# Kernel tuning notes

Hardware: AMD Instinct MI355X
Metric: run time of the kernel (lower is better)

Reference implementation:

```python
import jax, jax.numpy as jnp
import numpy as np

N_NODES = 50000
NNZ = 800000
NUM_EDGES = 10000
D = 128
EPS = 1e-8


def setup_inputs() -> dict:
    key = jax.random.key(0)
    k1, k2, k3, k4 = jax.random.split(key, 4)
    x = jax.random.normal(k1, (N_NODES, D), dtype=jnp.float32)
    node_ids = jax.random.randint(k2, (NNZ,), 0, N_NODES, dtype=jnp.int64)
    edge_ids = jax.random.randint(k3, (NNZ,), 0, NUM_EDGES, dtype=jnp.int64)
    hyperedge_index = jnp.stack([node_ids, edge_ids], axis=0)  # [2, nnz]
    # nn.Linear(in, out, bias=False) weight is [out, in]; kaiming-uniform-ish init
    bound = 1.0 / np.sqrt(D)
    W_node = jax.random.uniform(k4, (D, D), minval=-bound, maxval=bound, dtype=jnp.float32)
    bias = jnp.zeros((D,), dtype=jnp.float32)
    return {"x": x, "hyperedge_index": hyperedge_index, "W_node": W_node,
            "bias": bias, "num_hyperedges": NUM_EDGES}


def reference(x, hyperedge_index, W_node, bias, num_hyperedges):
    src = hyperedge_index[0]   # node ids, [nnz]
    edge = hyperedge_index[1]  # hyperedge ids, [nnz]
    N = x.shape[0]

    x_node = x @ W_node.T                                # [N, D]

    # node -> hyperedge mean
    edge_sum = jax.ops.segment_sum(x_node[src], edge, num_segments=num_hyperedges)
    node_counts = jax.ops.segment_sum(jnp.ones_like(edge, dtype=x.dtype), edge,
                                      num_segments=num_hyperedges)
    hyperedge_attr = edge_sum / (node_counts[:, None] + EPS)  # [E, D]

    # hyperedge -> node mean
    out = jax.ops.segment_sum(hyperedge_attr[edge], src, num_segments=N)
    degrees = jax.ops.segment_sum(jnp.ones_like(src, dtype=x.dtype), src,
                                  num_segments=N)
    out = out / (degrees[:, None] + EPS)                 # [N, D]

    return out + x_node + bias
```

## Files before the change

### kernel.cpp

```cpp
#include <hip/hip_runtime.h>

#define D 128
#define EPS 1e-8f
#define E_NUM 10000
#define CAP_E 192
#define CAP_N 64
#define CHUNK 2048
#define EB2 625
#define NB2 782
#define TB 1407
#define CAPB_E 1536
#define CAPB_N 1280
#define NODE_BASE (EB2 * CAPB_E)
#define STAGE_TOTAL (NODE_BASE + NB2 * CAPB_N)

typedef __attribute__((ext_vector_type(8))) short bf16x8;
typedef __attribute__((ext_vector_type(4))) float f32x4;

__device__ __forceinline__ unsigned bf16rn(float f) {
  unsigned u = __float_as_uint(f);
  return (u + 0x7fffu + ((u >> 16) & 1u)) >> 16;
}
__device__ __forceinline__ unsigned bf16pack(float a, float b) {
  return bf16rn(a) | (bf16rn(b) << 16);
}
__device__ __forceinline__ float lof(unsigned u) { return __uint_as_float(u << 16); }
__device__ __forceinline__ float hif(unsigned u) { return __uint_as_float(u & 0xffff0000u); }

#define ACCQ(u) do { \
    x0 += lof((u).x); y0 += hif((u).x); x1 += lof((u).y); y1 += hif((u).y); \
    x2 += lof((u).z); y2 += hif((u).z); x3 += lof((u).w); y3 += hif((u).w); } while (0)

struct SmemGemm {
  unsigned short Wfrag[2048 * 8];
  unsigned short cbuf[4][16 * 136];
};
struct SmemScat {
  int h[TB];
  int cur[TB];
  int end_[TB];
};

__global__ __launch_bounds__(256) void k1_gemm_scatter(
    const float* __restrict__ x, const float* __restrict__ W,
    unsigned* __restrict__ xnb, const int* __restrict__ node_ids,
    const int* __restrict__ edge_ids, int* __restrict__ gcur,
    unsigned* __restrict__ stage, int nnz, int C, int N) {
  __shared__ union { SmemGemm g; SmemScat s; } sm;
  const int t = threadIdx.x;

  if ((int)blockIdx.x < C) {
    const int c = blockIdx.x;
    const int base = c * CHUNK;
    const int lim = min(base + CHUNK, nnz);
    unsigned pk[8], rk[8];
    #pragma unroll
    for (int r = 0; r < 8; ++r) {
      int i = base + t + r * 256;
      pk[r] = (i < lim)
          ? (((unsigned)edge_ids[i] << 16) | (unsigned)node_ids[i])
          : 0xffffffffu;
    }
    for (int j = t; j < TB; j += 256) sm.s.h[j] = 0;
    __syncthreads();
    #pragma unroll
    for (int r = 0; r < 8; ++r) {
      if (pk[r] != 0xffffffffu) {
        unsigned pe = atomicAdd(&sm.s.h[pk[r] >> 20], 1);
        unsigned pn = atomicAdd(&sm.s.h[EB2 + ((pk[r] & 0xffffu) >> 6)], 1);
        rk[r] = pe | (pn << 16);
      } else {
        rk[r] = 0;
      }
    }
    __syncthreads();
    for (int j = t; j < TB; j += 256) {
      int hc = sm.s.h[j];
      int rb, cap;
      if (j < EB2) { rb = j * CAPB_E; cap = CAPB_E; }
      else         { rb = NODE_BASE + (j - EB2) * CAPB_N; cap = CAPB_N; }
      int off = hc ? atomicAdd(&gcur[j], hc) : 0;
      sm.s.cur[j] = rb + off;
      sm.s.end_[j] = rb + cap;
    }
    __syncthreads();
    #pragma unroll
    for (int r = 0; r < 8; ++r) {
      if (pk[r] != 0xffffffffu) {
        int be = pk[r] >> 20;
        int bn = EB2 + ((pk[r] & 0xffffu) >> 6);
        int pe = sm.s.cur[be] + (int)(rk[r] & 0xffffu);
        if (pe < sm.s.end_[be]) stage[pe] = pk[r];
        int pn = sm.s.cur[bn] + (int)(rk[r] >> 16);
        if (pn < sm.s.end_[bn]) stage[pn] = (pk[r] << 16) | (pk[r] >> 16);
      }
    }
    return;
  }

  const int wid = t >> 6;
  const int lane = t & 63;
  const int m = lane & 15;
  const int q = lane >> 4;

  #pragma unroll
  for (int i = 0; i < 8; ++i) {
    int c2 = t + i * 256;
    int ctkt = c2 >> 6;
    int l2 = c2 & 63;
    int n = (ctkt >> 2) * 16 + (l2 & 15);
    int k = (ctkt & 3) * 32 + (l2 >> 4) * 8;
    float4 p = *(const float4*)&W[n * 128 + k];
    float4 r = *(const float4*)&W[n * 128 + k + 4];
    uint4 pkk = make_uint4(bf16pack(p.x, p.y), bf16pack(p.z, p.w),
                           bf16pack(r.x, r.y), bf16pack(r.z, r.w));
    *(uint4*)&sm.g.Wfrag[c2 * 8] = pkk;
  }
  __syncthreads();

  const int blockRow = ((int)blockIdx.x - C) * 128;
  #pragma unroll
  for (int s = 0; s < 2; ++s) {
    const int row0 = blockRow + wid * 32 + s * 16;
    if (row0 >= N) break;

    bf16x8 a[4];
    #pragma unroll
    for (int kt = 0; kt < 4; ++kt) {
      int k0 = kt * 32 + q * 8;
      float4 p = *(const float4*)&x[(size_t)(row0 + m) * 128 + k0];
      float4 r = *(const float4*)&x[(size_t)(row0 + m) * 128 + k0 + 4];
      union { bf16x8 v; uint4 u; } au;
      au.u = make_uint4(bf16pack(p.x, p.y), bf16pack(p.z, p.w),
                        bf16pack(r.x, r.y), bf16pack(r.z, r.w));
      a[kt] = au.v;
    }

    #pragma unroll
    for (int ct = 0; ct < 8; ++ct) {
      f32x4 acc = {0.f, 0.f, 0.f, 0.f};
      #pragma unroll
      for (int kt = 0; kt < 4; ++kt) {
        bf16x8 b = *(const bf16x8*)&sm.g.Wfrag[((ct * 4 + kt) * 64 + lane) * 8];
        acc = __builtin_amdgcn_mfma_f32_16x16x32_bf16(a[kt], b, acc, 0, 0, 0);
      }
      #pragma unroll
      for (int r = 0; r < 4; ++r)
        sm.g.cbuf[wid][(q * 4 + r) * 136 + ct * 16 + m] =
            (unsigned short)bf16rn(acc[r]);
    }

    #pragma unroll
    for (int pass = 0; pass < 4; ++pass) {
      int chunk = pass * 64 + lane;
      int row = chunk >> 4;
      int cc = chunk & 15;
      uint4 v = *(const uint4*)&sm.g.cbuf[wid][row * 136 + cc * 8];
      *(uint4*)&xnb[(size_t)(row0 + row) * 64 + cc * 4] = v;
    }
  }
}

__global__ __launch_bounds__(512) void fuse_edge(
    const unsigned* __restrict__ stage, const int* __restrict__ gcur,
    const unsigned* __restrict__ xnb, unsigned* __restrict__ eattr) {
  __shared__ __align__(16) unsigned short lists[16 * CAP_E];
  __shared__ int lc[16];
  int b = blockIdx.x, t = threadIdx.x;
  if (t < 16) lc[t] = 0;
  __syncthreads();
  int total = gcur[b];
  if (total > CAPB_E) total = CAPB_E;
  const unsigned* seg = stage + (size_t)b * CAPB_E;
  for (int i = t; i < total; i += 512) {
    unsigned pkv = seg[i];
    int e = pkv >> 16;
    int p = atomicAdd(&lc[e & 15], 1);
    if (p < CAP_E) lists[(e & 15) * CAP_E + p] = (unsigned short)(pkv & 0xffffu);
  }
  __syncthreads();

  const int wid = t >> 6, lane = t & 63;
  const int h2 = lane >> 4, w = lane & 15;
  const uint4* X4 = (const uint4*)xnb;
  #pragma unroll
  for (int rep = 0; rep < 2; ++rep) {
    int j = wid + rep * 8;
    int e = (b << 4) + j;
    int c = lc[j];
    if (c > CAP_E) c = CAP_E;
    const unsigned short* lst = &lists[j * CAP_E];
    float x0=0,y0=0,x1=0,y1=0,x2=0,y2=0,x3=0,y3=0;
    int m2 = 0;
    #pragma unroll 2
    for (; m2 + 16 <= c; m2 += 16) {
      int i0 = lst[m2 + h2],     i1 = lst[m2 + 4 + h2],
          i2 = lst[m2 + 8 + h2], i3 = lst[m2 + 12 + h2];
      uint4 u0 = X4[(size_t)i0 * 16 + w];
      uint4 u1 = X4[(size_t)i1 * 16 + w];
      uint4 u2 = X4[(size_t)i2 * 16 + w];
      uint4 u3 = X4[(size_t)i3 * 16 + w];
      ACCQ(u0); ACCQ(u1); ACCQ(u2); ACCQ(u3);
    }
    for (; m2 < c; m2 += 4) {
      int ii = m2 + h2;
      int id = lst[ii < c ? ii : m2];
      uint4 u = X4[(size_t)id * 16 + w];
      if (ii < c) ACCQ(u);
    }
    x0 += __shfl_xor(x0, 16); y0 += __shfl_xor(y0, 16);
    x1 += __shfl_xor(x1, 16); y1 += __shfl_xor(y1, 16);
    x2 += __shfl_xor(x2, 16); y2 += __shfl_xor(y2, 16);
    x3 += __shfl_xor(x3, 16); y3 += __shfl_xor(y3, 16);
    x0 += __shfl_xor(x0, 32); y0 += __shfl_xor(y0, 32);
    x1 += __shfl_xor(x1, 32); y1 += __shfl_xor(y1, 32);
    x2 += __shfl_xor(x2, 32); y2 += __shfl_xor(y2, 32);
    x3 += __shfl_xor(x3, 32); y3 += __shfl_xor(y3, 32);
    if (lane < 16) {
      float inv = 1.f / ((float)c + EPS);
      uint4 o = make_uint4(bf16pack(x0 * inv, y0 * inv), bf16pack(x1 * inv, y1 * inv),
                           bf16pack(x2 * inv, y2 * inv), bf16pack(x3 * inv, y3 * inv));
      ((uint4*)eattr)[(size_t)e * 16 + w] = o;
    }
  }
}

__global__ __launch_bounds__(512) void fuse_node(
    const unsigned* __restrict__ stage, const int* __restrict__ gcur,
    const unsigned* __restrict__ eattr, const unsigned* __restrict__ xnb,
    const float* __restrict__ bias, float* __restrict__ out, int N) {
  __shared__ __align__(16) unsigned short lists[64 * CAP_N];
  __shared__ int lc[64];
  int b = blockIdx.x, t = threadIdx.x;
  if (t < 64) lc[t] = 0;
  __syncthreads();
  int total = gcur[EB2 + b];
  if (total > CAPB_N) total = CAPB_N;
  const unsigned* seg = stage + NODE_BASE + (size_t)b * CAPB_N;
  for (int i = t; i < total; i += 512) {
    unsigned pkv = seg[i];
    int n = pkv >> 16;
    int p = atomicAdd(&lc[n & 63], 1);
    if (p < CAP_N) lists[(n & 63) * CAP_N + p] = (unsigned short)(pkv & 0xffffu);
  }
  __syncthreads();

  const int wid = t >> 6, lane = t & 63;
  const int h2 = lane >> 4, w = lane & 15;
  const uint4* E4 = (const uint4*)eattr;
  const uint4* X4n = (const uint4*)xnb;
  const float4* B4 = (const float4*)bias;
  float4 bv0 = B4[2 * w], bv1 = B4[2 * w + 1];
  #pragma unroll
  for (int rep = 0; rep < 8; ++rep) {
    int j = wid + rep * 8;
    int v = (b << 6) + j;
    if (v >= N) continue;
    int c = lc[j];
    if (c > CAP_N) c = CAP_N;
    const unsigned short* lst = &lists[j * CAP_N];
    uint4 xr = X4n[(size_t)v * 16 + w];
    float x0=0,y0=0,x1=0,y1=0,x2=0,y2=0,x3=0,y3=0;
    int m2 = 0;
    for (; m2 + 16 <= c; m2 += 16) {
      int i0 = lst[m2 + h2],     i1 = lst[m2 + 4 + h2],
          i2 = lst[m2 + 8 + h2], i3 = lst[m2 + 12 + h2];
      uint4 u0 = E4[(size_t)i0 * 16 + w];
      uint4 u1 = E4[(size_t)i1 * 16 + w];
      uint4 u2 = E4[(size_t)i2 * 16 + w];
      uint4 u3 = E4[(size_t)i3 * 16 + w];
      ACCQ(u0); ACCQ(u1); ACCQ(u2); ACCQ(u3);
    }
    for (; m2 < c; m2 += 4) {
      int ii = m2 + h2;
      int id = lst[ii < c ? ii : m2];
      uint4 u = E4[(size_t)id * 16 + w];
      if (ii < c) ACCQ(u);
    }
    x0 += __shfl_xor(x0, 16); y0 += __shfl_xor(y0, 16);
    x1 += __shfl_xor(x1, 16); y1 += __shfl_xor(y1, 16);
    x2 += __shfl_xor(x2, 16); y2 += __shfl_xor(y2, 16);
    x3 += __shfl_xor(x3, 16); y3 += __shfl_xor(y3, 16);
    x0 += __shfl_xor(x0, 32); y0 += __shfl_xor(y0, 32);
    x1 += __shfl_xor(x1, 32); y1 += __shfl_xor(y1, 32);
    x2 += __shfl_xor(x2, 32); y2 += __shfl_xor(y2, 32);
    x3 += __shfl_xor(x3, 32); y3 += __shfl_xor(y3, 32);
    if (lane < 16) {
      float inv = 1.f / ((float)c + EPS);
      float4 o0 = make_float4(x0 * inv + lof(xr.x) + bv0.x,
                              y0 * inv + hif(xr.x) + bv0.y,
                              x1 * inv + lof(xr.y) + bv0.z,
                              y1 * inv + hif(xr.y) + bv0.w);
      float4 o1 = make_float4(x2 * inv + lof(xr.z) + bv1.x,
                              y2 * inv + hif(xr.z) + bv1.y,
                              x3 * inv + lof(xr.w) + bv1.z,
                              y3 * inv + hif(xr.w) + bv1.w);
      float4* orow = (float4*)(out + (size_t)v * D);
      orow[2 * w] = o0;
      orow[2 * w + 1] = o1;
    }
  }
}

extern "C" void kernel_launch(void* const* d_in, const int* in_sizes, int n_in,
                              void* d_out, int out_size, void* d_ws, size_t ws_size,
                              hipStream_t stream) {
  const float* x = (const float*)d_in[0];
  const int* hidx = (const int*)d_in[1];
  const float* W = (const float*)d_in[2];
  const float* bias = (const float*)d_in[3];

  const int N = in_sizes[0] / D;
  const int nnz = in_sizes[1] / 2;
  const int* node_ids = hidx;
  const int* edge_ids = hidx + nnz;
  const int C = (nnz + CHUNK - 1) / CHUNK;
  const int GB = (N + 127) / 128;

  int* ib = (int*)d_ws;
  int* gcur = ib;
  unsigned* stage = (unsigned*)(ib + 2048);
  unsigned* xnb = (unsigned*)(ib + 2048 + STAGE_TOTAL);
  unsigned* eattr = xnb + (size_t)N * 64;

  (void)hipMemsetAsync(gcur, 0, TB * sizeof(int), stream);

  k1_gemm_scatter<<<C + GB, 256, 0, stream>>>(x, W, xnb, node_ids, edge_ids,
                                              gcur, stage, nnz, C, N);

  fuse_edge<<<EB2, 512, 0, stream>>>(stage, gcur, xnb, eattr);

  fuse_node<<<NB2, 512, 0, stream>>>(stage, gcur, eattr, xnb, bias,
                                     (float*)d_out, N);
}
```

Measured before the change: 164.3 us.

## Build node adjacency lists concurrently with edge aggregation kernel

Moves the per-node list bucketing out of fuse_node and into extra blocks of the edge aggregation kernel, which write counts and lists to global memory. The node-side gather kernel then reads the prebuilt lists directly and no longer spends a phase on shared-memory atomics and a barrier. This lets list construction overlap the edge gather, which the fuse_node kernel would otherwise wait on. In exchange it adds a global write and re-read of the lists and more workspace use.

```diff
diff --git a/kernel.cpp b/kernel.cpp
--- a/kernel.cpp
+++ b/kernel.cpp
@@ -161,13 +161,38 @@
   }
 }
 
-__global__ __launch_bounds__(512) void fuse_edge(
+struct SmemFe { unsigned short lists[16 * CAP_E]; int lc[16]; };
+struct SmemNb { unsigned short lists[64 * CAP_N]; int lc[64]; };
+
+__global__ __launch_bounds__(512) void fe_nbuild(
     const unsigned* __restrict__ stage, const int* __restrict__ gcur,
-    const unsigned* __restrict__ xnb, unsigned* __restrict__ eattr) {
-  __shared__ __align__(16) unsigned short lists[16 * CAP_E];
-  __shared__ int lc[16];
-  int b = blockIdx.x, t = threadIdx.x;
-  if (t < 16) lc[t] = 0;
+    const unsigned* __restrict__ xnb, unsigned* __restrict__ eattr,
+    int* __restrict__ ncnt, unsigned short* __restrict__ nlist) {
+  __shared__ __align__(16) union { SmemFe fe; SmemNb nb; } sm;
+  const int b = blockIdx.x, t = threadIdx.x;
+
+  if (b >= EB2) {
+    const int b2 = b - EB2;
+    if (t < 64) sm.nb.lc[t] = 0;
+    __syncthreads();
+    int total = gcur[EB2 + b2];
+    if (total > CAPB_N) total = CAPB_N;
+    const unsigned* seg = stage + NODE_BASE + (size_t)b2 * CAPB_N;
+    for (int i = t; i < total; i += 512) {
+      unsigned pkv = seg[i];
+      int n = pkv >> 16;
+      int p = atomicAdd(&sm.nb.lc[n & 63], 1);
+      if (p < CAP_N) sm.nb.lists[(n & 63) * CAP_N + p] = (unsigned short)(pkv & 0xffffu);
+    }
+    __syncthreads();
+    if (t < 64) ncnt[(b2 << 6) + t] = min(sm.nb.lc[t], CAP_N);
+    const unsigned* src = (const unsigned*)sm.nb.lists;
+    unsigned* dst = (unsigned*)(nlist + ((size_t)b2 << 6) * CAP_N);
+    for (int i = t; i < 2048; i += 512) dst[i] = src[i];
+    return;
+  }
+
+  if (t < 16) sm.fe.lc[t] = 0;
   __syncthreads();
   int total = gcur[b];
   if (total > CAPB_E) total = CAPB_E;
@@ -175,8 +200,8 @@
   for (int i = t; i < total; i += 512) {
     unsigned pkv = seg[i];
     int e = pkv >> 16;
-    int p = atomicAdd(&lc[e & 15], 1);
-    if (p < CAP_E) lists[(e & 15) * CAP_E + p] = (unsigned short)(pkv & 0xffffu);
+    int p = atomicAdd(&sm.fe.lc[e & 15], 1);
+    if (p < CAP_E) sm.fe.lists[(e & 15) * CAP_E + p] = (unsigned short)(pkv & 0xffffu);
   }
   __syncthreads();
 
@@ -187,9 +212,9 @@
   for (int rep = 0; rep < 2; ++rep) {
     int j = wid + rep * 8;
     int e = (b << 4) + j;
-    int c = lc[j];
+    int c = sm.fe.lc[j];
     if (c > CAP_E) c = CAP_E;
-    const unsigned short* lst = &lists[j * CAP_E];
+    const unsigned short* lst = &sm.fe.lists[j * CAP_E];
     float x0=0,y0=0,x1=0,y1=0,x2=0,y2=0,x3=0,y3=0;
     int m2 = 0;
     #pragma unroll 2
@@ -226,25 +251,10 @@
 }
 
 __global__ __launch_bounds__(512) void fuse_node(
-    const unsigned* __restrict__ stage, const int* __restrict__ gcur,
+    const int* __restrict__ ncnt, const unsigned short* __restrict__ nlist,
     const unsigned* __restrict__ eattr, const unsigned* __restrict__ xnb,
     const float* __restrict__ bias, float* __restrict__ out, int N) {
-  __shared__ __align__(16) unsigned short lists[64 * CAP_N];
-  __shared__ int lc[64];
-  int b = blockIdx.x, t = threadIdx.x;
-  if (t < 64) lc[t] = 0;
-  __syncthreads();
-  int total = gcur[EB2 + b];
-  if (total > CAPB_N) total = CAPB_N;
-  const unsigned* seg = stage + NODE_BASE + (size_t)b * CAPB_N;
-  for (int i = t; i < total; i += 512) {
-    unsigned pkv = seg[i];
-    int n = pkv >> 16;
-    int p = atomicAdd(&lc[n & 63], 1);
-    if (p < CAP_N) lists[(n & 63) * CAP_N + p] = (unsigned short)(pkv & 0xffffu);
-  }
-  __syncthreads();
-
+  const int b = blockIdx.x, t = threadIdx.x;
   const int wid = t >> 6, lane = t & 63;
   const int h2 = lane >> 4, w = lane & 15;
   const uint4* E4 = (const uint4*)eattr;
@@ -256,9 +266,8 @@
     int j = wid + rep * 8;
     int v = (b << 6) + j;
     if (v >= N) continue;
-    int c = lc[j];
-    if (c > CAP_N) c = CAP_N;
-    const unsigned short* lst = &lists[j * CAP_N];
+    int c = ncnt[v];
+    const unsigned short* lst = nlist + (size_t)v * CAP_N;
     uint4 xr = X4n[(size_t)v * 16 + w];
     float x0=0,y0=0,x1=0,y1=0,x2=0,y2=0,x3=0,y3=0;
     int m2 = 0;
@@ -319,17 +328,19 @@
 
   int* ib = (int*)d_ws;
   int* gcur = ib;
-  unsigned* stage = (unsigned*)(ib + 2048);
-  unsigned* xnb = (unsigned*)(ib + 2048 + STAGE_TOTAL);
+  int* ncnt = ib + 2048;
+  unsigned* stage = (unsigned*)(ib + 53248);
+  unsigned* xnb = stage + STAGE_TOTAL;
   unsigned* eattr = xnb + (size_t)N * 64;
+  unsigned short* nlist = (unsigned short*)(eattr + (size_t)E_NUM * 64);
 
   (void)hipMemsetAsync(gcur, 0, TB * sizeof(int), stream);
 
   k1_gemm_scatter<<<C + GB, 256, 0, stream>>>(x, W, xnb, node_ids, edge_ids,
                                               gcur, stage, nnz, C, N);
 
-  fuse_edge<<<EB2, 512, 0, stream>>>(stage, gcur, xnb, eattr);
-
-  fuse_node<<<NB2, 512, 0, stream>>>(stage, gcur, eattr, xnb, bias,
+  fe_nbuild<<<TB, 512, 0, stream>>>(stage, gcur, xnb, eattr, ncnt, nlist);
+
+  fuse_node<<<NB2, 512, 0, stream>>>(ncnt, nlist, eattr, xnb, bias,
                                      (float*)d_out, N);
 }
```

Result: slower. 169.1 us (+3.0%).
